# Optimization experiments

Measured on AMD Instinct MI355X. Metric: run time of the kernel, lower is better.

Reference implementation:

```python
import jax, jax.numpy as jnp
import numpy as np

B, S, D = 8, 1024, 1024   # batch, routed-over rows, feature dim (input_dim)
E = 1024                  # output_dim (== S so gather indices are in range)
K = 2                     # top-k
ALPHA = 0.01


def setup_inputs() -> dict:
    key = jax.random.key(0)
    kx, kw = jax.random.split(key)
    x = jax.random.normal(kx, (B, S, D), dtype=jnp.float32)
    # nn.Linear(input_dim, output_dim, bias=False) weight: [E, D]
    W = jax.random.normal(kw, (E, D), dtype=jnp.float32) / np.sqrt(D).astype(np.float32)
    return {"x": x, "W": W}


def reference(x, W):
    # logits = proj(x): [B, S, E]  (temperature == 1.0 -> no scaling)
    logits = jnp.einsum('bsd,ed->bse', x, W)
    probs = jax.nn.softmax(logits, axis=-1)
    topk_probs, topk_idx = jax.lax.top_k(probs, K)            # [B, S, K]
    # router_selections: gather rows of x along dim 1 -> [B, S, K, D]
    sel = x[jnp.arange(B)[:, None, None], topk_idx]
    # y = sum_k topk_probs * selected rows -> [B, S, D]
    y = jnp.einsum('bsk,bskd->bsd', topk_probs, sel)
    # auxiliary load-balance loss
    router_probs = probs.mean(axis=(0, 1))                    # [E]
    counts = jnp.bincount(topk_idx.reshape(-1), length=E).astype(probs.dtype)
    router_fraction = counts / counts.sum()
    aux_loss = ALPHA * E * jnp.sum(router_probs * router_fraction)
    return y, aux_loss
```

## Files before the change

kernel.cpp:

```cpp
#include <hip/hip_runtime.h>

#define MTOK 8192
#define ED   1024

typedef short s16x8 __attribute__((ext_vector_type(8)));
typedef float f32x4 __attribute__((ext_vector_type(4)));
typedef int   i32x4 __attribute__((ext_vector_type(4)));
typedef unsigned short u16x4 __attribute__((ext_vector_type(4)));

__device__ __forceinline__ int cvtpk(float a, float b) {
    int r;
    asm("v_cvt_pk_bf16_f32 %0, %1, %2" : "=v"(r) : "v"(a), "v"(b));
    return r;
}

__device__ __forceinline__ void cvt_write(void* dstHi, void* dstLo,
                                          const float4 f0, const float4 f1) {
    i32x4 h, l;
    h[0] = cvtpk(f0.x, f0.y); h[1] = cvtpk(f0.z, f0.w);
    h[2] = cvtpk(f1.x, f1.y); h[3] = cvtpk(f1.z, f1.w);
    l[0] = cvtpk(f0.x - __builtin_bit_cast(float, h[0] << 16),
                 f0.y - __builtin_bit_cast(float, h[0] & 0xffff0000));
    l[1] = cvtpk(f0.z - __builtin_bit_cast(float, h[1] << 16),
                 f0.w - __builtin_bit_cast(float, h[1] & 0xffff0000));
    l[2] = cvtpk(f1.x - __builtin_bit_cast(float, h[2] << 16),
                 f1.y - __builtin_bit_cast(float, h[2] & 0xffff0000));
    l[3] = cvtpk(f1.z - __builtin_bit_cast(float, h[3] << 16),
                 f1.w - __builtin_bit_cast(float, h[3] & 0xffff0000));
    *(i32x4*)dstHi = h;
    *(i32x4*)dstLo = l;
}

__global__ __launch_bounds__(256) void frag_kernel(
        const float* __restrict__ M,
        unsigned short* __restrict__ Fhi, unsigned short* __restrict__ Flo) {
    const int task = blockIdx.x * 4 + (threadIdx.x >> 6);
    const int lane = threadIdx.x & 63;
    const int rowblk = task >> 5;
    const int kstep  = task & 31;
    const float* src = M + (size_t)(rowblk * 16 + (lane & 15)) * ED
                         + kstep * 32 + (lane >> 4) * 8;
    const float4 f0 = *(const float4*)src;
    const float4 f1 = *(const float4*)(src + 4);
    const size_t o = ((size_t)task * 64 + lane) * 8;
    cvt_write(&Fhi[o], &Flo[o], f0, f1);
}

__global__ __launch_bounds__(256, 2) void gemm_frag_kernel(
        const unsigned short* __restrict__ Ahi, const unsigned short* __restrict__ Alo,
        const unsigned short* __restrict__ Bhi, const unsigned short* __restrict__ Blo,
        float* __restrict__ C) {
    const int bid = blockIdx.x;
    const int xcd = bid & 7;
    const int j   = bid >> 3;
    const int bm  = xcd * 8 + (j >> 3);
    const int bn  = j & 7;

    const int lane = threadIdx.x & 63;
    const int wid  = threadIdx.x >> 6;
    const int wm = wid >> 1, wn = wid & 1;

    const size_t laneo = (size_t)lane * 8;
    const unsigned short* gAh = Ahi + (size_t)(bm * 8 + wm * 4) * 16384 + laneo;
    const unsigned short* gAl = Alo + (size_t)(bm * 8 + wm * 4) * 16384 + laneo;
    const unsigned short* gBh = Bhi + (size_t)(bn * 8 + wn * 4) * 16384 + laneo;
    const unsigned short* gBl = Blo + (size_t)(bn * 8 + wn * 4) * 16384 + laneo;

    s16x8 ah0[4], al0[4], bh0[4], bl0[4];
    s16x8 ah1[4], al1[4], bh1[4], bl1[4];

#define LOADSET(S, T)                                                  \
    _Pragma("unroll")                                                  \
    for (int i = 0; i < 4; ++i) {                                      \
        ah##S[i] = *(const s16x8*)(gAh + i * 16384 + (T) * 512);       \
        al##S[i] = *(const s16x8*)(gAl + i * 16384 + (T) * 512);       \
        bh##S[i] = *(const s16x8*)(gBh + i * 16384 + (T) * 512);       \
        bl##S[i] = *(const s16x8*)(gBl + i * 16384 + (T) * 512);       \
    }

#define MFMASET(S)                                                     \
    _Pragma("unroll")                                                  \
    for (int i = 0; i < 4; ++i)                                        \
        _Pragma("unroll")                                              \
        for (int jj = 0; jj < 4; ++jj) {                               \
            acc[i][jj] = __builtin_amdgcn_mfma_f32_16x16x32_bf16(ah##S[i], bh##S[jj], acc[i][jj], 0, 0, 0); \
            acc[i][jj] = __builtin_amdgcn_mfma_f32_16x16x32_bf16(ah##S[i], bl##S[jj], acc[i][jj], 0, 0, 0); \
            acc[i][jj] = __builtin_amdgcn_mfma_f32_16x16x32_bf16(al##S[i], bh##S[jj], acc[i][jj], 0, 0, 0); \
        }

    f32x4 acc[4][4] = {};

    LOADSET(0, 0);
    for (int t2 = 0; t2 < 32; t2 += 2) {
        LOADSET(1, t2 + 1);
        MFMASET(0);
        if (t2 + 2 < 32) LOADSET(0, t2 + 2);
        MFMASET(1);
    }
#undef LOADSET
#undef MFMASET

    const int fr = lane & 15, fg = lane >> 4;
    const int crow = bm * 128 + wm * 64 + fg * 4;
    const int ccol = bn * 128 + wn * 64 + fr;
#pragma unroll
    for (int i = 0; i < 4; ++i)
#pragma unroll
        for (int jj = 0; jj < 4; ++jj)
#pragma unroll
            for (int r = 0; r < 4; ++r)
                C[(size_t)(crow + i * 16 + r) * ED + ccol + jj * 16] = acc[i][jj][r];
}

#define BM 128
#define BN 128
#define BK 32
#define LDA (BM + 4)
#define LDB (BN + 4)

__global__ __launch_bounds__(256) void gemm_logits_kernel(const float* __restrict__ X,
                                                          const float* __restrict__ W,
                                                          float* __restrict__ C) {
    __shared__ float As[BK][LDA];
    __shared__ float Bs[BK][LDB];
    const int bm  = blockIdx.y * BM;
    const int bn  = blockIdx.x * BN;
    const int tid = threadIdx.x;
    const int tx  = tid & 15;
    const int ty  = tid >> 4;
    const int lr  = tid >> 3;
    const int lc  = (tid & 7) << 2;

    float acc[8][8];
#pragma unroll
    for (int i = 0; i < 8; ++i)
#pragma unroll
        for (int j = 0; j < 8; ++j) acc[i][j] = 0.f;

    for (int k0 = 0; k0 < ED; k0 += BK) {
#pragma unroll
        for (int i = 0; i < 4; ++i) {
            const int r = lr + i * 32;
            float4 va = *(const float4*)&X[(size_t)(bm + r) * ED + k0 + lc];
            As[lc + 0][r] = va.x; As[lc + 1][r] = va.y;
            As[lc + 2][r] = va.z; As[lc + 3][r] = va.w;
            float4 vb = *(const float4*)&W[(size_t)(bn + r) * ED + k0 + lc];
            Bs[lc + 0][r] = vb.x; Bs[lc + 1][r] = vb.y;
            Bs[lc + 2][r] = vb.z; Bs[lc + 3][r] = vb.w;
        }
        __syncthreads();
#pragma unroll
        for (int kk = 0; kk < BK; ++kk) {
            float a[8], b[8];
            *(float4*)&a[0] = *(const float4*)&As[kk][ty * 8];
            *(float4*)&a[4] = *(const float4*)&As[kk][ty * 8 + 4];
            *(float4*)&b[0] = *(const float4*)&Bs[kk][tx * 8];
            *(float4*)&b[4] = *(const float4*)&Bs[kk][tx * 8 + 4];
#pragma unroll
            for (int i = 0; i < 8; ++i)
#pragma unroll
                for (int j = 0; j < 8; ++j)
                    acc[i][j] = fmaf(a[i], b[j], acc[i][j]);
        }
        __syncthreads();
    }
#pragma unroll
    for (int i = 0; i < 8; ++i) {
        const int r = bm + ty * 8 + i;
        float4* dst = (float4*)&C[(size_t)r * ED + bn + tx * 8];
        dst[0] = make_float4(acc[i][0], acc[i][1], acc[i][2], acc[i][3]);
        dst[1] = make_float4(acc[i][4], acc[i][5], acc[i][6], acc[i][7]);
    }
}

__device__ __forceinline__ bool better(float v, int i, float bv, int bi) {
    return (v > bv) || (v == bv && i < bi);
}

__global__ __launch_bounds__(256, 8) void softmax_wave_kernel(
        const float* __restrict__ X, float* __restrict__ OUT,
        float* __restrict__ partial, int* __restrict__ counts) {
    __shared__ float L[4 * 1024];
    const int tid  = threadIdx.x;
    const int lane = tid & 63;
    const int w    = tid >> 6;
    const int t    = blockIdx.x * 4 + w;

    const float4* row4 = (const float4*)&OUT[(size_t)t * ED];
    float4 p[4];
#pragma unroll
    for (int i = 0; i < 4; ++i) p[i] = row4[lane + 64 * i];

    float v1 = -1e30f, v2 = -1e30f; int i1 = 0x7fffffff, i2 = 0x7fffffff;
#pragma unroll
    for (int i = 0; i < 4; ++i) {
        const float vv[4] = {p[i].x, p[i].y, p[i].z, p[i].w};
#pragma unroll
        for (int c = 0; c < 4; ++c) {
            const int e = 256 * i + 4 * lane + c;
            const float v = vv[c];
            if (better(v, e, v1, i1)) { v2 = v1; i2 = i1; v1 = v; i1 = e; }
            else if (better(v, e, v2, i2)) { v2 = v; i2 = e; }
        }
    }
#pragma unroll
    for (int off = 32; off; off >>= 1) {
        const float ov1 = __shfl_xor(v1, off); const int oi1 = __shfl_xor(i1, off);
        const float ov2 = __shfl_xor(v2, off); const int oi2 = __shfl_xor(i2, off);
        if (better(ov1, oi1, v1, i1)) {
            float nv2; int ni2;
            if (better(v1, i1, ov2, oi2)) { nv2 = v1; ni2 = i1; }
            else { nv2 = ov2; ni2 = oi2; }
            v1 = ov1; i1 = oi1; v2 = nv2; i2 = ni2;
        } else if (better(ov1, oi1, v2, i2)) { v2 = ov1; i2 = oi1; }
    }
    const float m = v1;

    float s = 0.f;
#pragma unroll
    for (int i = 0; i < 4; ++i) {
        p[i].x = __expf(p[i].x - m); p[i].y = __expf(p[i].y - m);
        p[i].z = __expf(p[i].z - m); p[i].w = __expf(p[i].w - m);
        s += p[i].x + p[i].y + p[i].z + p[i].w;
    }
#pragma unroll
    for (int off = 32; off; off >>= 1) s += __shfl_xor(s, off);
    const float inv = 1.f / s;

#pragma unroll
    for (int i = 0; i < 4; ++i) {
        float4 q = make_float4(p[i].x * inv, p[i].y * inv, p[i].z * inv, p[i].w * inv);
        *(float4*)&L[w * 1024 + i * 256 + lane * 4] = q;
    }

    const float p1 = inv;
    const float p2 = __expf(v2 - m) * inv;
    const int b = t >> 10;
    const float4* x1 = (const float4*)&X[((size_t)(b << 10) + i1) * ED];
    const float4* x2 = (const float4*)&X[((size_t)(b << 10) + i2) * ED];
    float4* yrow = (float4*)&OUT[(size_t)t * ED];
#pragma unroll
    for (int i = 0; i < 4; ++i) {
        const int idx = lane + 64 * i;
        const float4 a = x1[idx];
        const float4 c = x2[idx];
        float4 r;
        r.x = fmaf(p1, a.x, p2 * c.x);
        r.y = fmaf(p1, a.y, p2 * c.y);
        r.z = fmaf(p1, a.z, p2 * c.z);
        r.w = fmaf(p1, a.w, p2 * c.w);
        yrow[idx] = r;
    }

    if (lane == 0) { atomicAdd(&counts[i1], 1); atomicAdd(&counts[i2], 1); }

    __syncthreads();
    float4 s0 = *(float4*)&L[0 * 1024 + tid * 4];
    float4 s1 = *(float4*)&L[1 * 1024 + tid * 4];
    float4 s2 = *(float4*)&L[2 * 1024 + tid * 4];
    float4 s3 = *(float4*)&L[3 * 1024 + tid * 4];
    float4 r;
    r.x = (s0.x + s1.x) + (s2.x + s3.x);
    r.y = (s0.y + s1.y) + (s2.y + s3.y);
    r.z = (s0.z + s1.z) + (s2.z + s3.z);
    r.w = (s0.w + s1.w) + (s2.w + s3.w);
    *(float4*)&partial[(size_t)blockIdx.x * 1024 + tid * 4] = r;
}

__global__ __launch_bounds__(256) void aux1_kernel(const float* __restrict__ partial,
                                                   const int* __restrict__ counts,
                                                   float* __restrict__ dotPartial) {
    __shared__ float red[16][16];
    const int tid = threadIdx.x;
    const int el  = tid & 15;
    const int ch  = tid >> 4;
    const int e   = blockIdx.x * 16 + el;
    float s = 0.f;
    for (int k = 0; k < 128; ++k)
        s += partial[(size_t)(ch * 128 + k) * 1024 + e];
    red[ch][el] = s;
    __syncthreads();
    if (tid < 16) {
        float rs = 0.f;
#pragma unroll
        for (int c = 0; c < 16; ++c) rs += red[c][tid];
        float val = rs * (float)counts[blockIdx.x * 16 + tid];
#pragma unroll
        for (int off = 8; off; off >>= 1) val += __shfl_xor(val, off);
        if (tid == 0) dotPartial[blockIdx.x] = val;
    }
}

__global__ void aux2_kernel(const float* __restrict__ dotPartial, float* __restrict__ out) {
    const int lane = threadIdx.x;
    float v = dotPartial[lane];
#pragma unroll
    for (int off = 32; off; off >>= 1) v += __shfl_xor(v, off);
    if (lane == 0)
        out[(size_t)MTOK * ED] = v * (0.01f * 1024.f / (8192.f * 16384.f));
}

#define TOKS_PER_BLK 16
__global__ __launch_bounds__(256) void softmax_topk_y_kernel(
        const float* __restrict__ X, float* __restrict__ OUT,
        float* __restrict__ router_sum, int* __restrict__ counts) {
    __shared__ float routerLocal[ED];
    __shared__ float redMax[4];
    __shared__ float redSum[4];
    __shared__ float wV1[4]; __shared__ int wI1[4];
    __shared__ float wV2[4]; __shared__ int wI2[4];

    const int tid  = threadIdx.x;
    const int lane = tid & 63;
    const int wave = tid >> 6;

    for (int e = tid; e < ED; e += 256) routerLocal[e] = 0.f;
    __syncthreads();

    const int t0 = blockIdx.x * TOKS_PER_BLK;
    for (int t = t0; t < t0 + TOKS_PER_BLK; ++t) {
        const float* lrow = &OUT[(size_t)t * ED];
        float l[4];
#pragma unroll
        for (int i = 0; i < 4; ++i) l[i] = lrow[tid + i * 256];

        float m = fmaxf(fmaxf(l[0], l[1]), fmaxf(l[2], l[3]));
#pragma unroll
        for (int off = 32; off; off >>= 1) m = fmaxf(m, __shfl_xor(m, off));
        if (lane == 0) redMax[wave] = m;
        __syncthreads();
        m = fmaxf(fmaxf(redMax[0], redMax[1]), fmaxf(redMax[2], redMax[3]));

        float p[4]; float s = 0.f;
#pragma unroll
        for (int i = 0; i < 4; ++i) { p[i] = expf(l[i] - m); s += p[i]; }
#pragma unroll
        for (int off = 32; off; off >>= 1) s += __shfl_xor(s, off);
        if (lane == 0) redSum[wave] = s;

        float v1 = -1e30f, v2 = -1e30f; int i1 = 0x7fffffff, i2 = 0x7fffffff;
#pragma unroll
        for (int i = 0; i < 4; ++i) {
            const float v = l[i]; const int ix = tid + i * 256;
            if (better(v, ix, v1, i1)) { v2 = v1; i2 = i1; v1 = v; i1 = ix; }
            else if (better(v, ix, v2, i2)) { v2 = v; i2 = ix; }
        }
#pragma unroll
        for (int off = 32; off; off >>= 1) {
            const float ov1 = __shfl_xor(v1, off); const int oi1 = __shfl_xor(i1, off);
            const float ov2 = __shfl_xor(v2, off); const int oi2 = __shfl_xor(i2, off);
            if (better(ov1, oi1, v1, i1)) {
                float nv2; int ni2;
                if (better(v1, i1, ov2, oi2)) { nv2 = v1; ni2 = i1; }
                else { nv2 = ov2; ni2 = oi2; }
                v1 = ov1; i1 = oi1; v2 = nv2; i2 = ni2;
            } else if (better(ov1, oi1, v2, i2)) { v2 = ov1; i2 = oi1; }
        }
        if (lane == 0) { wV1[wave] = v1; wI1[wave] = i1; wV2[wave] = v2; wI2[wave] = i2; }
        __syncthreads();

        v1 = wV1[0]; i1 = wI1[0]; v2 = wV2[0]; i2 = wI2[0];
#pragma unroll
        for (int w = 1; w < 4; ++w) {
            const float ov1 = wV1[w]; const int oi1 = wI1[w];
            const float ov2 = wV2[w]; const int oi2 = wI2[w];
            if (better(ov1, oi1, v1, i1)) {
                float nv2; int ni2;
                if (better(v1, i1, ov2, oi2)) { nv2 = v1; ni2 = i1; }
                else { nv2 = ov2; ni2 = oi2; }
                v1 = ov1; i1 = oi1; v2 = nv2; i2 = ni2;
            } else if (better(ov1, oi1, v2, i2)) { v2 = ov1; i2 = oi1; }
        }
        const float stot = redSum[0] + redSum[1] + redSum[2] + redSum[3];
        const float inv = 1.f / stot;

#pragma unroll
        for (int i = 0; i < 4; ++i) routerLocal[tid + i * 256] += p[i] * inv;

        const float p1 = expf(v1 - m) * inv;
        const float p2 = expf(v2 - m) * inv;

        const int b = t >> 10;
        const float4* x1 = (const float4*)&X[((size_t)(b << 10) + i1) * ED];
        const float4* x2 = (const float4*)&X[((size_t)(b << 10) + i2) * ED];
        float4* yrow = (float4*)&OUT[(size_t)t * ED];
        const float4 a = x1[tid];
        const float4 c = x2[tid];
        float4 r;
        r.x = fmaf(p1, a.x, p2 * c.x);
        r.y = fmaf(p1, a.y, p2 * c.y);
        r.z = fmaf(p1, a.z, p2 * c.z);
        r.w = fmaf(p1, a.w, p2 * c.w);
        yrow[tid] = r;

        if (tid == 0) { atomicAdd(&counts[i1], 1); atomicAdd(&counts[i2], 1); }
        __syncthreads();
    }

    for (int e = tid; e < ED; e += 256) atomicAdd(&router_sum[e], routerLocal[e]);
}

__global__ __launch_bounds__(256) void aux_kernel(const float* __restrict__ router_sum,
                                                  const int* __restrict__ counts,
                                                  float* __restrict__ out) {
    __shared__ float red[4];
    const int tid = threadIdx.x;
    float s = 0.f;
    for (int e = tid; e < ED; e += 256)
        s += (router_sum[e] * (1.f / 8192.f)) * ((float)counts[e] * (1.f / 16384.f));
#pragma unroll
    for (int off = 32; off; off >>= 1) s += __shfl_xor(s, off);
    if ((tid & 63) == 0) red[tid >> 6] = s;
    __syncthreads();
    if (tid == 0) out[(size_t)MTOK * ED] = 0.01f * 1024.f * (red[0] + red[1] + red[2] + red[3]);
}

extern "C" void kernel_launch(void* const* d_in, const int* in_sizes, int n_in,
                              void* d_out, int out_size, void* d_ws, size_t ws_size,
                              hipStream_t stream) {
    const float* X = (const float*)d_in[0];
    const float* W = (const float*)d_in[1];
    float* out = (float*)d_out;

    const size_t WS_NEED = (size_t)MTOK * ED * 2 * sizeof(unsigned short)
                         + (size_t)ED * ED * 2 * sizeof(unsigned short)
                         + 64 * sizeof(float) + ED * sizeof(int);

    if (ws_size >= WS_NEED) {
        unsigned short* Xfh = (unsigned short*)d_ws;
        unsigned short* Xfl = Xfh + (size_t)MTOK * ED;
        unsigned short* Wfh = Xfl + (size_t)MTOK * ED;
        unsigned short* Wfl = Wfh + (size_t)ED * ED;
        float* dotPartial   = (float*)(Wfl + (size_t)ED * ED);
        int*   counts       = (int*)(dotPartial + 64);
        float* partial      = (float*)Xfh;

        hipMemsetAsync(counts, 0, ED * sizeof(int), stream);
        frag_kernel<<<4096, 256, 0, stream>>>(X, Xfh, Xfl);
        frag_kernel<<<512, 256, 0, stream>>>(W, Wfh, Wfl);
        gemm_frag_kernel<<<512, 256, 0, stream>>>(Xfh, Xfl, Wfh, Wfl, out);
        softmax_wave_kernel<<<MTOK / 4, 256, 0, stream>>>(X, out, partial, counts);
        aux1_kernel<<<64, 256, 0, stream>>>(partial, counts, dotPartial);
        aux2_kernel<<<1, 64, 0, stream>>>(dotPartial, out);
    } else {
        float* router_sum = (float*)d_ws;
        int*   counts     = (int*)((char*)d_ws + ED * sizeof(float));
        hipMemsetAsync(d_ws, 0, ED * (sizeof(float) + sizeof(int)), stream);
        dim3 ggrid(ED / BN, MTOK / BM);
        gemm_logits_kernel<<<ggrid, 256, 0, stream>>>(X, W, out);
        softmax_topk_y_kernel<<<MTOK / TOKS_PER_BLK, 256, 0, stream>>>(X, out, router_sum, counts);
        aux_kernel<<<1, 256, 0, stream>>>(router_sum, counts, out);
    }
}
```

Baseline: 108.6 us.

## Fuse logits GEMM, softmax, top-k and gather into one kernel

```diff
diff --git a/kernel.cpp b/kernel.cpp
--- a/kernel.cpp
+++ b/kernel.cpp
@@ -14,8 +14,8 @@
     return r;
 }
 
-__device__ __forceinline__ void cvt_write(void* dstHi, void* dstLo,
-                                          const float4 f0, const float4 f1) {
+__device__ __forceinline__ void cvt_regs(const float4 f0, const float4 f1,
+                                         s16x8* hi, s16x8* lo) {
     i32x4 h, l;
     h[0] = cvtpk(f0.x, f0.y); h[1] = cvtpk(f0.z, f0.w);
     h[2] = cvtpk(f1.x, f1.y); h[3] = cvtpk(f1.z, f1.w);
@@ -27,8 +27,16 @@
                  f1.y - __builtin_bit_cast(float, h[2] & 0xffff0000));
     l[3] = cvtpk(f1.z - __builtin_bit_cast(float, h[3] << 16),
                  f1.w - __builtin_bit_cast(float, h[3] & 0xffff0000));
-    *(i32x4*)dstHi = h;
-    *(i32x4*)dstLo = l;
+    *hi = __builtin_bit_cast(s16x8, h);
+    *lo = __builtin_bit_cast(s16x8, l);
+}
+
+__device__ __forceinline__ void cvt_write(void* dstHi, void* dstLo,
+                                          const float4 f0, const float4 f1) {
+    s16x8 h, l;
+    cvt_regs(f0, f1, &h, &l);
+    *(s16x8*)dstHi = h;
+    *(s16x8*)dstLo = l;
 }
 
 __global__ __launch_bounds__(256) void frag_kernel(
@@ -46,70 +54,205 @@
     cvt_write(&Fhi[o], &Flo[o], f0, f1);
 }
 
-__global__ __launch_bounds__(256, 2) void gemm_frag_kernel(
-        const unsigned short* __restrict__ Ahi, const unsigned short* __restrict__ Alo,
-        const unsigned short* __restrict__ Bhi, const unsigned short* __restrict__ Blo,
-        float* __restrict__ C) {
-    const int bid = blockIdx.x;
-    const int xcd = bid & 7;
-    const int j   = bid >> 3;
-    const int bm  = xcd * 8 + (j >> 3);
-    const int bn  = j & 7;
-
-    const int lane = threadIdx.x & 63;
-    const int wid  = threadIdx.x >> 6;
-    const int wm = wid >> 1, wn = wid & 1;
-
-    const size_t laneo = (size_t)lane * 8;
-    const unsigned short* gAh = Ahi + (size_t)(bm * 8 + wm * 4) * 16384 + laneo;
-    const unsigned short* gAl = Alo + (size_t)(bm * 8 + wm * 4) * 16384 + laneo;
-    const unsigned short* gBh = Bhi + (size_t)(bn * 8 + wn * 4) * 16384 + laneo;
-    const unsigned short* gBl = Blo + (size_t)(bn * 8 + wn * 4) * 16384 + laneo;
-
-    s16x8 ah0[4], al0[4], bh0[4], bl0[4];
-    s16x8 ah1[4], al1[4], bh1[4], bl1[4];
-
-#define LOADSET(S, T)                                                  \
-    _Pragma("unroll")                                                  \
-    for (int i = 0; i < 4; ++i) {                                      \
-        ah##S[i] = *(const s16x8*)(gAh + i * 16384 + (T) * 512);       \
-        al##S[i] = *(const s16x8*)(gAl + i * 16384 + (T) * 512);       \
-        bh##S[i] = *(const s16x8*)(gBh + i * 16384 + (T) * 512);       \
-        bl##S[i] = *(const s16x8*)(gBl + i * 16384 + (T) * 512);       \
-    }
-
-#define MFMASET(S)                                                     \
-    _Pragma("unroll")                                                  \
-    for (int i = 0; i < 4; ++i)                                        \
-        _Pragma("unroll")                                              \
-        for (int jj = 0; jj < 4; ++jj) {                               \
-            acc[i][jj] = __builtin_amdgcn_mfma_f32_16x16x32_bf16(ah##S[i], bh##S[jj], acc[i][jj], 0, 0, 0); \
-            acc[i][jj] = __builtin_amdgcn_mfma_f32_16x16x32_bf16(ah##S[i], bl##S[jj], acc[i][jj], 0, 0, 0); \
-            acc[i][jj] = __builtin_amdgcn_mfma_f32_16x16x32_bf16(al##S[i], bh##S[jj], acc[i][jj], 0, 0, 0); \
-        }
-
-    f32x4 acc[4][4] = {};
-
-    LOADSET(0, 0);
+__device__ __forceinline__ bool better(float v, int i, float bv, int bi) {
+    return (v > bv) || (v == bv && i < bi);
+}
+
+__global__ __launch_bounds__(512, 2) void moe_fused_kernel(
+        const float* __restrict__ X,
+        const unsigned short* __restrict__ Wfh, const unsigned short* __restrict__ Wfl,
+        float* __restrict__ OUT, float* __restrict__ partial,
+        int* __restrict__ counts) {
+    __shared__ float L[32 * 1024];
+
+    const int tid  = threadIdx.x;
+    const int lane = tid & 63;
+    const int w    = tid >> 6;
+    const int fr   = lane & 15, fg = lane >> 4;
+    const int tok0 = blockIdx.x * 32;
+
+    const float* gA = X + (size_t)(tok0 + fr) * ED + fg * 8;
+    const unsigned short* gBh = Wfh + (size_t)(w * 8) * 16384 + lane * 8;
+    const unsigned short* gBl = Wfl + (size_t)(w * 8) * 16384 + lane * 8;
+
+    f32x4 acc[2][8] = {};
+    s16x8 ah[2], al[2];
+    s16x8 bh0[8], bl0[8], bh1[8], bl1[8];
+
+#define LOADA(T)                                                        \
+    _Pragma("unroll")                                                   \
+    for (int rb = 0; rb < 2; ++rb) {                                    \
+        const float* s = gA + (size_t)(rb * 16) * ED + (T) * 32;        \
+        const float4 f0 = *(const float4*)s;                            \
+        const float4 f1 = *(const float4*)(s + 4);                      \
+        cvt_regs(f0, f1, &ah[rb], &al[rb]);                             \
+    }
+
+#define LOADB(S, T)                                                     \
+    _Pragma("unroll")                                                   \
+    for (int cb = 0; cb < 8; ++cb) {                                    \
+        bh##S[cb] = *(const s16x8*)(gBh + cb * 16384 + (T) * 512);      \
+        bl##S[cb] = *(const s16x8*)(gBl + cb * 16384 + (T) * 512);      \
+    }
+
+#define MFMAB(S)                                                        \
+    _Pragma("unroll")                                                   \
+    for (int rb = 0; rb < 2; ++rb)                                      \
+        _Pragma("unroll")                                               \
+        for (int cb = 0; cb < 8; ++cb) {                                \
+            acc[rb][cb] = __builtin_amdgcn_mfma_f32_16x16x32_bf16(ah[rb], bh##S[cb], acc[rb][cb], 0, 0, 0); \
+            acc[rb][cb] = __builtin_amdgcn_mfma_f32_16x16x32_bf16(ah[rb], bl##S[cb], acc[rb][cb], 0, 0, 0); \
+            acc[rb][cb] = __builtin_amdgcn_mfma_f32_16x16x32_bf16(al[rb], bh##S[cb], acc[rb][cb], 0, 0, 0); \
+        }
+
+    LOADA(0);
+    LOADB(0, 0);
     for (int t2 = 0; t2 < 32; t2 += 2) {
-        LOADSET(1, t2 + 1);
-        MFMASET(0);
-        if (t2 + 2 < 32) LOADSET(0, t2 + 2);
-        MFMASET(1);
-    }
-#undef LOADSET
-#undef MFMASET
-
-    const int fr = lane & 15, fg = lane >> 4;
-    const int crow = bm * 128 + wm * 64 + fg * 4;
-    const int ccol = bn * 128 + wn * 64 + fr;
+        LOADB(1, t2 + 1);
+        MFMAB(0);
+        LOADA(t2 + 1);
+        if (t2 + 2 < 32) LOADB(0, t2 + 2);
+        MFMAB(1);
+        if (t2 + 2 < 32) LOADA(t2 + 2);
+    }
+#undef LOADA
+#undef LOADB
+#undef MFMAB
+
+#pragma unroll
+    for (int rb = 0; rb < 2; ++rb)
+#pragma unroll
+        for (int cb = 0; cb < 8; ++cb)
+#pragma unroll
+            for (int r = 0; r < 4; ++r)
+                L[(rb * 16 + fg * 4 + r) * 1024 + w * 128 + cb * 16 + fr] = acc[rb][cb][r];
+    __syncthreads();
+
+    float4 rl[4];
+#pragma unroll
+    for (int i = 0; i < 4; ++i) rl[i] = make_float4(0.f, 0.f, 0.f, 0.f);
+
+    for (int q = 0; q < 4; ++q) {
+        const int tk = w * 4 + q;
+        float4 p[4];
+#pragma unroll
+        for (int i = 0; i < 4; ++i)
+            p[i] = *(const float4*)&L[tk * 1024 + i * 256 + lane * 4];
+
+        float v1 = -1e30f, v2 = -1e30f; int i1 = 0x7fffffff, i2 = 0x7fffffff;
+#pragma unroll
+        for (int i = 0; i < 4; ++i) {
+            const float vv[4] = {p[i].x, p[i].y, p[i].z, p[i].w};
+#pragma unroll
+            for (int c = 0; c < 4; ++c) {
+                const int e = 256 * i + 4 * lane + c;
+                const float v = vv[c];
+                if (better(v, e, v1, i1)) { v2 = v1; i2 = i1; v1 = v; i1 = e; }
+                else if (better(v, e, v2, i2)) { v2 = v; i2 = e; }
+            }
+        }
+#pragma unroll
+        for (int off = 32; off; off >>= 1) {
+            const float ov1 = __shfl_xor(v1, off); const int oi1 = __shfl_xor(i1, off);
+            const float ov2 = __shfl_xor(v2, off); const int oi2 = __shfl_xor(i2, off);
+            if (better(ov1, oi1, v1, i1)) {
+                float nv2; int ni2;
+                if (better(v1, i1, ov2, oi2)) { nv2 = v1; ni2 = i1; }
+                else { nv2 = ov2; ni2 = oi2; }
+                v1 = ov1; i1 = oi1; v2 = nv2; i2 = ni2;
+            } else if (better(ov1, oi1, v2, i2)) { v2 = ov1; i2 = oi1; }
+        }
+        const float m = v1;
+
+        float s = 0.f;
+#pragma unroll
+        for (int i = 0; i < 4; ++i) {
+            p[i].x = __expf(p[i].x - m); p[i].y = __expf(p[i].y - m);
+            p[i].z = __expf(p[i].z - m); p[i].w = __expf(p[i].w - m);
+            s += p[i].x + p[i].y + p[i].z + p[i].w;
+        }
+#pragma unroll
+        for (int off = 32; off; off >>= 1) s += __shfl_xor(s, off);
+        const float inv = 1.f / s;
+
+#pragma unroll
+        for (int i = 0; i < 4; ++i) {
+            rl[i].x += p[i].x * inv; rl[i].y += p[i].y * inv;
+            rl[i].z += p[i].z * inv; rl[i].w += p[i].w * inv;
+        }
+
+        const float p1 = inv;
+        const float p2 = __expf(v2 - m) * inv;
+        const int tglob = tok0 + tk;
+        const int b = tglob >> 10;
+        const float4* x1 = (const float4*)&X[((size_t)(b << 10) + i1) * ED];
+        const float4* x2 = (const float4*)&X[((size_t)(b << 10) + i2) * ED];
+        float4* yrow = (float4*)&OUT[(size_t)tglob * ED];
+#pragma unroll
+        for (int i = 0; i < 4; ++i) {
+            const int idx = lane + 64 * i;
+            const float4 a = x1[idx];
+            const float4 c = x2[idx];
+            float4 r;
+            r.x = fmaf(p1, a.x, p2 * c.x);
+            r.y = fmaf(p1, a.y, p2 * c.y);
+            r.z = fmaf(p1, a.z, p2 * c.z);
+            r.w = fmaf(p1, a.w, p2 * c.w);
+            yrow[idx] = r;
+        }
+        if (lane == 0) { atomicAdd(&counts[i1], 1); atomicAdd(&counts[i2], 1); }
+    }
+
 #pragma unroll
     for (int i = 0; i < 4; ++i)
-#pragma unroll
-        for (int jj = 0; jj < 4; ++jj)
-#pragma unroll
-            for (int r = 0; r < 4; ++r)
-                C[(size_t)(crow + i * 16 + r) * ED + ccol + jj * 16] = acc[i][jj][r];
+        *(float4*)&L[(w * 4 + i) * 1024 + i * 256 + lane * 4] = rl[i];
+    __syncthreads();
+
+    {
+        const int e = tid * 2;
+        const int i = e >> 8;
+        float s0 = 0.f, s1 = 0.f;
+#pragma unroll
+        for (int ww = 0; ww < 8; ++ww) {
+            s0 += L[(ww * 4 + i) * 1024 + e];
+            s1 += L[(ww * 4 + i) * 1024 + e + 1];
+        }
+        partial[(size_t)blockIdx.x * 1024 + e]     = s0;
+        partial[(size_t)blockIdx.x * 1024 + e + 1] = s1;
+    }
+}
+
+__global__ __launch_bounds__(256) void aux1_kernel(const float* __restrict__ partial,
+                                                   const int* __restrict__ counts,
+                                                   float* __restrict__ dotPartial) {
+    __shared__ float red[16][16];
+    const int tid = threadIdx.x;
+    const int el  = tid & 15;
+    const int ch  = tid >> 4;
+    const int e   = blockIdx.x * 16 + el;
+    float s = 0.f;
+    for (int k = 0; k < 16; ++k)
+        s += partial[(size_t)(ch * 16 + k) * 1024 + e];
+    red[ch][el] = s;
+    __syncthreads();
+    if (tid < 16) {
+        float rs = 0.f;
+#pragma unroll
+        for (int c = 0; c < 16; ++c) rs += red[c][tid];
+        float val = rs * (float)counts[blockIdx.x * 16 + tid];
+#pragma unroll
+        for (int off = 8; off; off >>= 1) val += __shfl_xor(val, off);
+        if (tid == 0) dotPartial[blockIdx.x] = val;
+    }
+}
+
+__global__ void aux2_kernel(const float* __restrict__ dotPartial, float* __restrict__ out) {
+    const int lane = threadIdx.x;
+    float v = dotPartial[lane];
+#pragma unroll
+    for (int off = 32; off; off >>= 1) v += __shfl_xor(v, off);
+    if (lane == 0)
+        out[(size_t)MTOK * ED] = v * (0.01f * 1024.f / (8192.f * 16384.f));
 }
 
 #define BM 128
@@ -173,133 +316,6 @@
     }
 }
 
-__device__ __forceinline__ bool better(float v, int i, float bv, int bi) {
-    return (v > bv) || (v == bv && i < bi);
-}
-
-__global__ __launch_bounds__(256, 8) void softmax_wave_kernel(
-        const float* __restrict__ X, float* __restrict__ OUT,
-        float* __restrict__ partial, int* __restrict__ counts) {
-    __shared__ float L[4 * 1024];
-    const int tid  = threadIdx.x;
-    const int lane = tid & 63;
-    const int w    = tid >> 6;
-    const int t    = blockIdx.x * 4 + w;
-
-    const float4* row4 = (const float4*)&OUT[(size_t)t * ED];
-    float4 p[4];
-#pragma unroll
-    for (int i = 0; i < 4; ++i) p[i] = row4[lane + 64 * i];
-
-    float v1 = -1e30f, v2 = -1e30f; int i1 = 0x7fffffff, i2 = 0x7fffffff;
-#pragma unroll
-    for (int i = 0; i < 4; ++i) {
-        const float vv[4] = {p[i].x, p[i].y, p[i].z, p[i].w};
-#pragma unroll
-        for (int c = 0; c < 4; ++c) {
-            const int e = 256 * i + 4 * lane + c;
-            const float v = vv[c];
-            if (better(v, e, v1, i1)) { v2 = v1; i2 = i1; v1 = v; i1 = e; }
-            else if (better(v, e, v2, i2)) { v2 = v; i2 = e; }
-        }
-    }
-#pragma unroll
-    for (int off = 32; off; off >>= 1) {
-        const float ov1 = __shfl_xor(v1, off); const int oi1 = __shfl_xor(i1, off);
-        const float ov2 = __shfl_xor(v2, off); const int oi2 = __shfl_xor(i2, off);
-        if (better(ov1, oi1, v1, i1)) {
-            float nv2; int ni2;
-            if (better(v1, i1, ov2, oi2)) { nv2 = v1; ni2 = i1; }
-            else { nv2 = ov2; ni2 = oi2; }
-            v1 = ov1; i1 = oi1; v2 = nv2; i2 = ni2;
-        } else if (better(ov1, oi1, v2, i2)) { v2 = ov1; i2 = oi1; }
-    }
-    const float m = v1;
-
-    float s = 0.f;
-#pragma unroll
-    for (int i = 0; i < 4; ++i) {
-        p[i].x = __expf(p[i].x - m); p[i].y = __expf(p[i].y - m);
-        p[i].z = __expf(p[i].z - m); p[i].w = __expf(p[i].w - m);
-        s += p[i].x + p[i].y + p[i].z + p[i].w;
-    }
-#pragma unroll
-    for (int off = 32; off; off >>= 1) s += __shfl_xor(s, off);
-    const float inv = 1.f / s;
-
-#pragma unroll
-    for (int i = 0; i < 4; ++i) {
-        float4 q = make_float4(p[i].x * inv, p[i].y * inv, p[i].z * inv, p[i].w * inv);
-        *(float4*)&L[w * 1024 + i * 256 + lane * 4] = q;
-    }
-
-    const float p1 = inv;
-    const float p2 = __expf(v2 - m) * inv;
-    const int b = t >> 10;
-    const float4* x1 = (const float4*)&X[((size_t)(b << 10) + i1) * ED];
-    const float4* x2 = (const float4*)&X[((size_t)(b << 10) + i2) * ED];
-    float4* yrow = (float4*)&OUT[(size_t)t * ED];
-#pragma unroll
-    for (int i = 0; i < 4; ++i) {
-        const int idx = lane + 64 * i;
-        const float4 a = x1[idx];
-        const float4 c = x2[idx];
-        float4 r;
-        r.x = fmaf(p1, a.x, p2 * c.x);
-        r.y = fmaf(p1, a.y, p2 * c.y);
-        r.z = fmaf(p1, a.z, p2 * c.z);
-        r.w = fmaf(p1, a.w, p2 * c.w);
-        yrow[idx] = r;
-    }
-
-    if (lane == 0) { atomicAdd(&counts[i1], 1); atomicAdd(&counts[i2], 1); }
-
-    __syncthreads();
-    float4 s0 = *(float4*)&L[0 * 1024 + tid * 4];
-    float4 s1 = *(float4*)&L[1 * 1024 + tid * 4];
-    float4 s2 = *(float4*)&L[2 * 1024 + tid * 4];
-    float4 s3 = *(float4*)&L[3 * 1024 + tid * 4];
-    float4 r;
-    r.x = (s0.x + s1.x) + (s2.x + s3.x);
-    r.y = (s0.y + s1.y) + (s2.y + s3.y);
-    r.z = (s0.z + s1.z) + (s2.z + s3.z);
-    r.w = (s0.w + s1.w) + (s2.w + s3.w);
-    *(float4*)&partial[(size_t)blockIdx.x * 1024 + tid * 4] = r;
-}
-
-__global__ __launch_bounds__(256) void aux1_kernel(const float* __restrict__ partial,
-                                                   const int* __restrict__ counts,
-                                                   float* __restrict__ dotPartial) {
-    __shared__ float red[16][16];
-    const int tid = threadIdx.x;
-    const int el  = tid & 15;
-    const int ch  = tid >> 4;
-    const int e   = blockIdx.x * 16 + el;
-    float s = 0.f;
-    for (int k = 0; k < 128; ++k)
-        s += partial[(size_t)(ch * 128 + k) * 1024 + e];
-    red[ch][el] = s;
-    __syncthreads();
-    if (tid < 16) {
-        float rs = 0.f;
-#pragma unroll
-        for (int c = 0; c < 16; ++c) rs += red[c][tid];
-        float val = rs * (float)counts[blockIdx.x * 16 + tid];
-#pragma unroll
-        for (int off = 8; off; off >>= 1) val += __shfl_xor(val, off);
-        if (tid == 0) dotPartial[blockIdx.x] = val;
-    }
-}
-
-__global__ void aux2_kernel(const float* __restrict__ dotPartial, float* __restrict__ out) {
-    const int lane = threadIdx.x;
-    float v = dotPartial[lane];
-#pragma unroll
-    for (int off = 32; off; off >>= 1) v += __shfl_xor(v, off);
-    if (lane == 0)
-        out[(size_t)MTOK * ED] = v * (0.01f * 1024.f / (8192.f * 16384.f));
-}
-
 #define TOKS_PER_BLK 16
 __global__ __launch_bounds__(256) void softmax_topk_y_kernel(
         const float* __restrict__ X, float* __restrict__ OUT,
@@ -422,24 +438,20 @@
     const float* W = (const float*)d_in[1];
     float* out = (float*)d_out;
 
-    const size_t WS_NEED = (size_t)MTOK * ED * 2 * sizeof(unsigned short)
-                         + (size_t)ED * ED * 2 * sizeof(unsigned short)
+    const size_t WS_NEED = (size_t)ED * ED * 2 * sizeof(unsigned short)
+                         + (size_t)256 * 1024 * sizeof(float)
                          + 64 * sizeof(float) + ED * sizeof(int);
 
     if (ws_size >= WS_NEED) {
-        unsigned short* Xfh = (unsigned short*)d_ws;
-        unsigned short* Xfl = Xfh + (size_t)MTOK * ED;
-        unsigned short* Wfh = Xfl + (size_t)MTOK * ED;
+        unsigned short* Wfh = (unsigned short*)d_ws;
         unsigned short* Wfl = Wfh + (size_t)ED * ED;
-        float* dotPartial   = (float*)(Wfl + (size_t)ED * ED);
+        float* partial      = (float*)(Wfl + (size_t)ED * ED);
+        float* dotPartial   = partial + (size_t)256 * 1024;
         int*   counts       = (int*)(dotPartial + 64);
-        float* partial      = (float*)Xfh;
 
         hipMemsetAsync(counts, 0, ED * sizeof(int), stream);
-        frag_kernel<<<4096, 256, 0, stream>>>(X, Xfh, Xfl);
         frag_kernel<<<512, 256, 0, stream>>>(W, Wfh, Wfl);
-        gemm_frag_kernel<<<512, 256, 0, stream>>>(Xfh, Xfl, Wfh, Wfl, out);
-        softmax_wave_kernel<<<MTOK / 4, 256, 0, stream>>>(X, out, partial, counts);
+        moe_fused_kernel<<<MTOK / 32, 512, 0, stream>>>(X, Wfh, Wfl, out, partial, counts);
         aux1_kernel<<<64, 256, 0, stream>>>(partial, counts, dotPartial);
         aux2_kernel<<<1, 64, 0, stream>>>(dotPartial, out);
     } else {
```

Measured after the change: 95.20 us. 12.3% less time.

## Fuse X bf16 hi/lo split into GEMM and drop X fragment pre-pass

Applied to the files above, without the earlier changes.

```diff
diff --git a/kernel.cpp b/kernel.cpp
--- a/kernel.cpp
+++ b/kernel.cpp
@@ -14,21 +14,21 @@
     return r;
 }
 
-__device__ __forceinline__ void cvt_write(void* dstHi, void* dstLo,
-                                          const float4 f0, const float4 f1) {
+__device__ __forceinline__ void cvt_regs(const f32x4 f0, const f32x4 f1,
+                                         s16x8* hi, s16x8* lo) {
     i32x4 h, l;
-    h[0] = cvtpk(f0.x, f0.y); h[1] = cvtpk(f0.z, f0.w);
-    h[2] = cvtpk(f1.x, f1.y); h[3] = cvtpk(f1.z, f1.w);
-    l[0] = cvtpk(f0.x - __builtin_bit_cast(float, h[0] << 16),
-                 f0.y - __builtin_bit_cast(float, h[0] & 0xffff0000));
-    l[1] = cvtpk(f0.z - __builtin_bit_cast(float, h[1] << 16),
-                 f0.w - __builtin_bit_cast(float, h[1] & 0xffff0000));
-    l[2] = cvtpk(f1.x - __builtin_bit_cast(float, h[2] << 16),
-                 f1.y - __builtin_bit_cast(float, h[2] & 0xffff0000));
-    l[3] = cvtpk(f1.z - __builtin_bit_cast(float, h[3] << 16),
-                 f1.w - __builtin_bit_cast(float, h[3] & 0xffff0000));
-    *(i32x4*)dstHi = h;
-    *(i32x4*)dstLo = l;
+    h[0] = cvtpk(f0[0], f0[1]); h[1] = cvtpk(f0[2], f0[3]);
+    h[2] = cvtpk(f1[0], f1[1]); h[3] = cvtpk(f1[2], f1[3]);
+    l[0] = cvtpk(f0[0] - __builtin_bit_cast(float, h[0] << 16),
+                 f0[1] - __builtin_bit_cast(float, h[0] & 0xffff0000));
+    l[1] = cvtpk(f0[2] - __builtin_bit_cast(float, h[1] << 16),
+                 f0[3] - __builtin_bit_cast(float, h[1] & 0xffff0000));
+    l[2] = cvtpk(f1[0] - __builtin_bit_cast(float, h[2] << 16),
+                 f1[1] - __builtin_bit_cast(float, h[2] & 0xffff0000));
+    l[3] = cvtpk(f1[2] - __builtin_bit_cast(float, h[3] << 16),
+                 f1[3] - __builtin_bit_cast(float, h[3] & 0xffff0000));
+    *hi = __builtin_bit_cast(s16x8, h);
+    *lo = __builtin_bit_cast(s16x8, l);
 }
 
 __global__ __launch_bounds__(256) void frag_kernel(
@@ -40,14 +40,26 @@
     const int kstep  = task & 31;
     const float* src = M + (size_t)(rowblk * 16 + (lane & 15)) * ED
                          + kstep * 32 + (lane >> 4) * 8;
-    const float4 f0 = *(const float4*)src;
-    const float4 f1 = *(const float4*)(src + 4);
+    const f32x4 f0 = *(const f32x4*)src;
+    const f32x4 f1 = *(const f32x4*)(src + 4);
+    s16x8 h, l;
+    cvt_regs(f0, f1, &h, &l);
     const size_t o = ((size_t)task * 64 + lane) * 8;
-    cvt_write(&Fhi[o], &Flo[o], f0, f1);
-}
-
-__global__ __launch_bounds__(256, 2) void gemm_frag_kernel(
-        const unsigned short* __restrict__ Ahi, const unsigned short* __restrict__ Alo,
+    *(s16x8*)&Fhi[o] = h;
+    *(s16x8*)&Flo[o] = l;
+}
+
+#define GLOADF(dst, ptr) \
+    asm volatile("global_load_dwordx4 %0, %1, off" : "=v"(dst) : "v"(ptr))
+#define GLOADS(dst, ptr) \
+    asm volatile("global_load_dwordx4 %0, %1, off" : "=v"(dst) : "v"(ptr))
+#define WAIT16() do { asm volatile("s_waitcnt vmcnt(16)" ::: "memory"); \
+                      __builtin_amdgcn_sched_barrier(0); } while (0)
+#define WAIT0()  do { asm volatile("s_waitcnt vmcnt(0)" ::: "memory");  \
+                      __builtin_amdgcn_sched_barrier(0); } while (0)
+
+__global__ __launch_bounds__(256, 2) void gemm_asm_kernel(
+        const float* __restrict__ Xf,
         const unsigned short* __restrict__ Bhi, const unsigned short* __restrict__ Blo,
         float* __restrict__ C) {
     const int bid = blockIdx.x;
@@ -59,48 +71,65 @@
     const int lane = threadIdx.x & 63;
     const int wid  = threadIdx.x >> 6;
     const int wm = wid >> 1, wn = wid & 1;
-
-    const size_t laneo = (size_t)lane * 8;
-    const unsigned short* gAh = Ahi + (size_t)(bm * 8 + wm * 4) * 16384 + laneo;
-    const unsigned short* gAl = Alo + (size_t)(bm * 8 + wm * 4) * 16384 + laneo;
-    const unsigned short* gBh = Bhi + (size_t)(bn * 8 + wn * 4) * 16384 + laneo;
-    const unsigned short* gBl = Blo + (size_t)(bn * 8 + wn * 4) * 16384 + laneo;
-
-    s16x8 ah0[4], al0[4], bh0[4], bl0[4];
-    s16x8 ah1[4], al1[4], bh1[4], bl1[4];
-
-#define LOADSET(S, T)                                                  \
-    _Pragma("unroll")                                                  \
-    for (int i = 0; i < 4; ++i) {                                      \
-        ah##S[i] = *(const s16x8*)(gAh + i * 16384 + (T) * 512);       \
-        al##S[i] = *(const s16x8*)(gAl + i * 16384 + (T) * 512);       \
-        bh##S[i] = *(const s16x8*)(gBh + i * 16384 + (T) * 512);       \
-        bl##S[i] = *(const s16x8*)(gBl + i * 16384 + (T) * 512);       \
-    }
-
-#define MFMASET(S)                                                     \
-    _Pragma("unroll")                                                  \
-    for (int i = 0; i < 4; ++i)                                        \
-        _Pragma("unroll")                                              \
-        for (int jj = 0; jj < 4; ++jj) {                               \
-            acc[i][jj] = __builtin_amdgcn_mfma_f32_16x16x32_bf16(ah##S[i], bh##S[jj], acc[i][jj], 0, 0, 0); \
-            acc[i][jj] = __builtin_amdgcn_mfma_f32_16x16x32_bf16(ah##S[i], bl##S[jj], acc[i][jj], 0, 0, 0); \
-            acc[i][jj] = __builtin_amdgcn_mfma_f32_16x16x32_bf16(al##S[i], bh##S[jj], acc[i][jj], 0, 0, 0); \
-        }
+    const int fr = lane & 15, fg = lane >> 4;
+
+    const float* gA = Xf + (size_t)(bm * 128 + wm * 64 + fr) * ED + fg * 8;
+    const unsigned short* gBh = Bhi + (size_t)(bn * 8 + wn * 4) * 16384 + (size_t)lane * 8;
+    const unsigned short* gBl = Blo + (size_t)(bn * 8 + wn * 4) * 16384 + (size_t)lane * 8;
+
+    f32x4 aR0[8], aR1[8];
+    s16x8 bh0[4], bl0[4], bh1[4], bl1[4];
+
+#define LOADALL(S, T)                                                       \
+    {                                                                       \
+        _Pragma("unroll")                                                   \
+        for (int i = 0; i < 4; ++i) {                                       \
+            const float* p = gA + (size_t)(i * 16) * ED + (T) * 32;         \
+            GLOADF(aR##S[2 * i],     p);                                    \
+            GLOADF(aR##S[2 * i + 1], p + 4);                                \
+        }                                                                   \
+        _Pragma("unroll")                                                   \
+        for (int i = 0; i < 4; ++i) {                                       \
+            GLOADS(bh##S[i], gBh + i * 16384 + (T) * 512);                  \
+            GLOADS(bl##S[i], gBl + i * 16384 + (T) * 512);                  \
+        }                                                                   \
+    }
+
+#define COMPUTE(S)                                                          \
+    {                                                                       \
+        s16x8 ah[4], al[4];                                                 \
+        _Pragma("unroll")                                                   \
+        for (int i = 0; i < 4; ++i)                                         \
+            cvt_regs(aR##S[2 * i], aR##S[2 * i + 1], &ah[i], &al[i]);       \
+        _Pragma("unroll")                                                   \
+        for (int i = 0; i < 4; ++i)                                         \
+            _Pragma("unroll")                                               \
+            for (int jj = 0; jj < 4; ++jj) {                                \
+                acc[i][jj] = __builtin_amdgcn_mfma_f32_16x16x32_bf16(ah[i], bh##S[jj], acc[i][jj], 0, 0, 0); \
+                acc[i][jj] = __builtin_amdgcn_mfma_f32_16x16x32_bf16(ah[i], bl##S[jj], acc[i][jj], 0, 0, 0); \
+                acc[i][jj] = __builtin_amdgcn_mfma_f32_16x16x32_bf16(al[i], bh##S[jj], acc[i][jj], 0, 0, 0); \
+            }                                                               \
+    }
 
     f32x4 acc[4][4] = {};
 
-    LOADSET(0, 0);
-    for (int t2 = 0; t2 < 32; t2 += 2) {
-        LOADSET(1, t2 + 1);
-        MFMASET(0);
-        if (t2 + 2 < 32) LOADSET(0, t2 + 2);
-        MFMASET(1);
-    }
-#undef LOADSET
-#undef MFMASET
-
-    const int fr = lane & 15, fg = lane >> 4;
+    LOADALL(0, 0);
+    for (int t2 = 0; t2 < 30; t2 += 2) {
+        LOADALL(1, t2 + 1);
+        WAIT16();
+        COMPUTE(0);
+        LOADALL(0, t2 + 2);
+        WAIT16();
+        COMPUTE(1);
+    }
+    LOADALL(1, 31);
+    WAIT16();
+    COMPUTE(0);
+    WAIT0();
+    COMPUTE(1);
+#undef LOADALL
+#undef COMPUTE
+
     const int crow = bm * 128 + wm * 64 + fg * 4;
     const int ccol = bn * 128 + wn * 64 + fr;
 #pragma unroll
@@ -422,23 +451,20 @@
     const float* W = (const float*)d_in[1];
     float* out = (float*)d_out;
 
-    const size_t WS_NEED = (size_t)MTOK * ED * 2 * sizeof(unsigned short)
-                         + (size_t)ED * ED * 2 * sizeof(unsigned short)
+    const size_t WS_NEED = (size_t)ED * ED * 2 * sizeof(unsigned short)
+                         + (size_t)2048 * 1024 * sizeof(float)
                          + 64 * sizeof(float) + ED * sizeof(int);
 
     if (ws_size >= WS_NEED) {
-        unsigned short* Xfh = (unsigned short*)d_ws;
-        unsigned short* Xfl = Xfh + (size_t)MTOK * ED;
-        unsigned short* Wfh = Xfl + (size_t)MTOK * ED;
+        unsigned short* Wfh = (unsigned short*)d_ws;
         unsigned short* Wfl = Wfh + (size_t)ED * ED;
-        float* dotPartial   = (float*)(Wfl + (size_t)ED * ED);
+        float* partial      = (float*)(Wfl + (size_t)ED * ED);
+        float* dotPartial   = partial + (size_t)2048 * 1024;
         int*   counts       = (int*)(dotPartial + 64);
-        float* partial      = (float*)Xfh;
 
         hipMemsetAsync(counts, 0, ED * sizeof(int), stream);
-        frag_kernel<<<4096, 256, 0, stream>>>(X, Xfh, Xfl);
         frag_kernel<<<512, 256, 0, stream>>>(W, Wfh, Wfl);
-        gemm_frag_kernel<<<512, 256, 0, stream>>>(Xfh, Xfl, Wfh, Wfl, out);
+        gemm_asm_kernel<<<512, 256, 0, stream>>>(X, Wfh, Wfl, out);
         softmax_wave_kernel<<<MTOK / 4, 256, 0, stream>>>(X, out, partial, counts);
         aux1_kernel<<<64, 256, 0, stream>>>(partial, counts, dotPartial);
         aux2_kernel<<<1, 64, 0, stream>>>(dotPartial, out);
```

Result: slower. 119.4 us (+10.0%).
